# Kernel tuning notes

Hardware: AMD Instinct MI355X
Metric: run time of the kernel (lower is better)

## Reference

```python
import jax, jax.numpy as jnp
import numpy as np

_CODEBOOK = np.array([
 [-1,-1,-1,-1,-1,-1,-1,-1,-1,-1],[-1,-1,-1,-1,1,1,-1,-1,-1,1],[-1,-1,-1,1,-1,-1,-1,-1,1,1],[-1,-1,-1,1,1,1,-1,-1,1,-1],
 [-1,-1,1,-1,-1,-1,-1,1,1,-1],[-1,-1,1,-1,1,1,-1,1,1,1],[-1,-1,1,1,-1,-1,-1,1,-1,1],[-1,-1,1,1,1,1,-1,1,-1,-1],
 [-1,1,-1,-1,-1,-1,1,1,-1,-1],[-1,1,-1,-1,1,1,1,1,-1,1],[-1,1,-1,1,-1,-1,1,1,1,1],[-1,1,-1,1,1,1,1,1,1,-1],
 [-1,1,1,-1,-1,-1,1,-1,1,-1],[-1,1,1,-1,1,1,1,-1,1,1],[-1,1,1,1,-1,-1,1,-1,-1,1],[-1,1,1,1,1,1,1,-1,-1,-1],
 [1,-1,-1,-1,-1,1,1,-1,-1,-1],[1,-1,-1,-1,1,-1,1,-1,-1,1],[1,-1,-1,1,-1,1,1,-1,1,1],[1,-1,-1,1,1,-1,1,-1,1,-1],
 [1,-1,1,-1,-1,1,1,1,1,-1],[1,-1,1,-1,1,-1,1,1,1,1],[1,-1,1,1,-1,1,1,1,-1,1],[1,-1,1,1,1,-1,1,1,-1,-1],
 [1,1,-1,-1,-1,1,-1,1,-1,-1],[1,1,-1,-1,1,-1,-1,1,-1,1],[1,1,-1,1,-1,1,-1,1,1,1],[1,1,-1,1,1,-1,-1,1,1,-1],
 [1,1,1,-1,-1,1,-1,-1,1,-1],[1,1,1,-1,1,-1,-1,-1,1,1],[1,1,1,1,-1,1,-1,-1,-1,1],[1,1,1,1,1,-1,-1,-1,-1,-1]],
 dtype=np.float32)

def setup_inputs() -> dict:
    key = jax.random.key(0)
    B, N, D = 64, 65536, 10
    signal = jax.random.normal(key, (B, N, D), dtype=jnp.float32)
    codebook = jnp.asarray(_CODEBOOK)  # [32, 10]
    return {"signal": signal, "codebook": codebook}

def reference(signal, codebook):
    # Euclidean distances to all 32 codewords via Gram trick: [B, N, 32]
    x2 = jnp.sum(signal * signal, axis=-1, keepdims=True)          # [B, N, 1]
    c2 = jnp.sum(codebook * codebook, axis=-1)                      # [32]
    xc = jnp.einsum('bnd,kd->bnk', signal, codebook)                # [B, N, 32]
    d2 = jnp.maximum(x2 + c2 - 2.0 * xc, 0.0)
    distances = jnp.sqrt(d2)
    soft_assignments = jax.nn.softmax(-distances, axis=2)           # [B, N, 32]
    most_like = jnp.argmax(soft_assignments, axis=2)                # [B, N]
    softdecision = codebook[most_like]                              # [B, N, 10]
    return softdecision
```

## Files before the change

kernel.cpp:

```cpp
#include <hip/hip_runtime.h>
#include <stdint.h>

#define PTS    256
#define DIM    10
#define STRIDE 11
#define NVEC   ((PTS * DIM) / 4)

__device__ constexpr float CB[32][10] = {
 {-1,-1,-1,-1,-1,-1,-1,-1,-1,-1},{-1,-1,-1,-1,1,1,-1,-1,-1,1},{-1,-1,-1,1,-1,-1,-1,-1,1,1},{-1,-1,-1,1,1,1,-1,-1,1,-1},
 {-1,-1,1,-1,-1,-1,-1,1,1,-1},{-1,-1,1,-1,1,1,-1,1,1,1},{-1,-1,1,1,-1,-1,-1,1,-1,1},{-1,-1,1,1,1,1,-1,1,-1,-1},
 {-1,1,-1,-1,-1,-1,1,1,-1,-1},{-1,1,-1,-1,1,1,1,1,-1,1},{-1,1,-1,1,-1,-1,1,1,1,1},{-1,1,-1,1,1,1,1,1,1,-1},
 {-1,1,1,-1,-1,-1,1,-1,1,-1},{-1,1,1,-1,1,1,1,-1,1,1},{-1,1,1,1,-1,-1,1,-1,-1,1},{-1,1,1,1,1,1,1,-1,-1,-1},
 {1,-1,-1,-1,-1,1,1,-1,-1,-1},{1,-1,-1,-1,1,-1,1,-1,-1,1},{1,-1,-1,1,-1,1,1,-1,1,1},{1,-1,-1,1,1,-1,1,-1,1,-1},
 {1,-1,1,-1,-1,1,1,1,1,-1},{1,-1,1,-1,1,-1,1,1,1,1},{1,-1,1,1,-1,1,1,1,-1,1},{1,-1,1,1,1,-1,1,1,-1,-1},
 {1,1,-1,-1,-1,1,-1,1,-1,-1},{1,1,-1,-1,1,-1,-1,1,-1,1},{1,1,-1,1,-1,1,-1,1,1,1},{1,1,-1,1,1,-1,-1,1,1,-1},
 {1,1,1,-1,-1,1,-1,-1,1,-1},{1,1,1,-1,1,-1,-1,-1,1,1},{1,1,1,1,-1,1,-1,-1,-1,1},{1,1,1,1,1,-1,-1,-1,-1,-1}};

__global__ __launch_bounds__(PTS) void softdec_kernel(
    const float* __restrict__ sig, float* __restrict__ out)
{
    __shared__ float sIn [PTS * STRIDE];
    __shared__ float sOut[PTS * STRIDE];
    const int tid = threadIdx.x;
    const size_t base = (size_t)blockIdx.x * (PTS * DIM);

    const float4* __restrict__ gin = (const float4*)(sig + base);
    #pragma unroll
    for (int it = 0; it < 3; ++it) {
        const int i = tid + it * PTS;
        if (i < NVEC) {
            const float4 v = gin[i];
            const float vv[4] = {v.x, v.y, v.z, v.w};
            #pragma unroll
            for (int j = 0; j < 4; ++j) {
                const int gg = i * 4 + j;
                const int p  = gg / DIM;
                const int c  = gg - p * DIM;
                sIn[p * STRIDE + c] = vv[j];
            }
        }
    }
    __syncthreads();

    float x[DIM];
    #pragma unroll
    for (int j = 0; j < DIM; ++j) x[j] = sIn[tid * STRIDE + j];

    float best = -1e30f;
    int   bi   = 0;
    #pragma unroll
    for (int k = 0; k < 32; ++k) {
        float s = 0.0f;
        #pragma unroll
        for (int j = 0; j < DIM; ++j)
            s = (CB[k][j] > 0.0f) ? (s + x[j]) : (s - x[j]);
        if (s > best) { best = s; bi = k; }
    }

    #pragma unroll
    for (int j = 0; j < DIM; ++j)
        sOut[tid * STRIDE + j] = CB[bi][j];
    __syncthreads();

    float4* __restrict__ gout = (float4*)(out + base);
    #pragma unroll
    for (int it = 0; it < 3; ++it) {
        const int i = tid + it * PTS;
        if (i < NVEC) {
            float4 v;
            float* vv = (float*)&v;
            #pragma unroll
            for (int j = 0; j < 4; ++j) {
                const int gg = i * 4 + j;
                const int p  = gg / DIM;
                const int c  = gg - p * DIM;
                vv[j] = sOut[p * STRIDE + c];
            }
            gout[i] = v;
        }
    }
}

extern "C" void kernel_launch(void* const* d_in, const int* in_sizes, int n_in,
                              void* d_out, int out_size, void* d_ws, size_t ws_size,
                              hipStream_t stream) {
    const float* sig = (const float*)d_in[0];
    float* out = (float*)d_out;
    const int total  = in_sizes[0];
    const int pts    = total / DIM;
    const int blocks = pts / PTS;
    softdec_kernel<<<blocks, PTS, 0, stream>>>(sig, out);
}
```

Before: 278.2 us.

## Replace brute-force codeword search with factored decoder and direct vector loads

Replaces the 32x10 sign-sum search with a factored decoder that shares partial sums across codewords. It evaluates 16 candidate pairs and resolves the last bit with an absolute value and sign test. Each thread now processes two points with five 16-byte loads and stores straight from registers, removing the LDS staging buffers and both barriers. The per-thread strided vector accesses may coalesce less well than the old layout, and the result relies on the codebook's specific structure.

Measured after the change: 284.7 us. +2.4%, slower.

```diff
diff --git a/kernel.cpp b/kernel.cpp
--- a/kernel.cpp
+++ b/kernel.cpp
@@ -1,84 +1,101 @@
 #include <hip/hip_runtime.h>
 #include <stdint.h>
 
-#define PTS    256
-#define DIM    10
-#define STRIDE 11
-#define NVEC   ((PTS * DIM) / 4)
+#define THREADS 256
+#define DIM     10
 
-__device__ constexpr float CB[32][10] = {
- {-1,-1,-1,-1,-1,-1,-1,-1,-1,-1},{-1,-1,-1,-1,1,1,-1,-1,-1,1},{-1,-1,-1,1,-1,-1,-1,-1,1,1},{-1,-1,-1,1,1,1,-1,-1,1,-1},
- {-1,-1,1,-1,-1,-1,-1,1,1,-1},{-1,-1,1,-1,1,1,-1,1,1,1},{-1,-1,1,1,-1,-1,-1,1,-1,1},{-1,-1,1,1,1,1,-1,1,-1,-1},
- {-1,1,-1,-1,-1,-1,1,1,-1,-1},{-1,1,-1,-1,1,1,1,1,-1,1},{-1,1,-1,1,-1,-1,1,1,1,1},{-1,1,-1,1,1,1,1,1,1,-1},
- {-1,1,1,-1,-1,-1,1,-1,1,-1},{-1,1,1,-1,1,1,1,-1,1,1},{-1,1,1,1,-1,-1,1,-1,-1,1},{-1,1,1,1,1,1,1,-1,-1,-1},
- {1,-1,-1,-1,-1,1,1,-1,-1,-1},{1,-1,-1,-1,1,-1,1,-1,-1,1},{1,-1,-1,1,-1,1,1,-1,1,1},{1,-1,-1,1,1,-1,1,-1,1,-1},
- {1,-1,1,-1,-1,1,1,1,1,-1},{1,-1,1,-1,1,-1,1,1,1,1},{1,-1,1,1,-1,1,1,1,-1,1},{1,-1,1,1,1,-1,1,1,-1,-1},
- {1,1,-1,-1,-1,1,-1,1,-1,-1},{1,1,-1,-1,1,-1,-1,1,-1,1},{1,1,-1,1,-1,1,-1,1,1,1},{1,1,-1,1,1,-1,-1,1,1,-1},
- {1,1,1,-1,-1,1,-1,-1,1,-1},{1,1,1,-1,1,-1,-1,-1,1,1},{1,1,1,1,-1,1,-1,-1,-1,1},{1,1,1,1,1,-1,-1,-1,-1,-1}};
+typedef float v4f __attribute__((ext_vector_type(4)));
 
-__global__ __launch_bounds__(PTS) void softdec_kernel(
+
+__device__ __forceinline__ void decide10(const float* __restrict__ x,
+                                         float* __restrict__ y)
+{
+    const float x0=x[0], x1=x[1], x2=x[2], x3=x[3], x4=x[4];
+    const float x5=x[5], x6=x[6], x7=x[7], x8=x[8], x9=x[9];
+
+    const float GP = x1 - x7, GM = x1 + x7;
+    const float JP = x2 - x8, JM = x2 + x8;
+    const float LP = x3 - x9, LM = x3 + x9;
+
+    const float K11 =  LP + x4;
+    const float K10 =  LM - x4;
+    const float K01 =  x4 - LP;
+    const float K00 = -LM - x4;
+
+    const float H111 = JP + K11, H110 = JP + K10, H101 = JM + K01, H100 = JM + K00;
+    const float H011 = K11 - JP, H010 = K10 - JP, H001 = K01 - JM, H000 = K00 - JM;
+
+    float r[16];
+    r[15] = GP + H111; r[14] = GP + H110; r[13] = GP + H101; r[12] = GP + H100;
+    r[11] = GM + H011; r[10] = GM + H010; r[ 9] = GM + H001; r[ 8] = GM + H000;
+    r[ 7] = H111 - GP; r[ 6] = H110 - GP; r[ 5] = H101 - GP; r[ 4] = H100 - GP;
+    r[ 3] = H011 - GM; r[ 2] = H010 - GM; r[ 1] = H001 - GM; r[ 0] = H000 - GM;
+
+    const float p56 = x5 + x6, m56 = x5 - x6;
+    const float S11 = x0 - p56;
+    const float S10 = x0 + m56;
+    const float S01 = x0 - m56;
+    const float S00 = x0 + p56;
+    const float A11 = fabsf(S11), A10 = fabsf(S10), A01 = fabsf(S01), A00 = fabsf(S00);
+
+    float m[16];
+    #pragma unroll
+    for (int i = 0; i < 16; ++i) {
+        const bool b3 = (i >> 3) & 1, b0 = i & 1;
+        const float A = b3 ? (b0 ? A11 : A10) : (b0 ? A01 : A00);
+        m[i] = r[i] + A;
+    }
+
+    float best = m[0];
+    int   bi   = 0;
+    #pragma unroll
+    for (int i = 1; i < 16; ++i) {
+        const bool c = m[i] > best;
+        best = c ? m[i] : best;
+        bi   = c ? i    : bi;
+    }
+
+    const int wb3 = (bi >> 3) & 1, wb0 = bi & 1;
+    const float Sw = wb3 ? (wb0 ? S11 : S10) : (wb0 ? S01 : S00);
+    const float s4 = (Sw > 0.0f) ? 1.0f : -1.0f;
+    const float s0 = (bi & 1) ? 1.0f : -1.0f;
+    const float s1 = (bi & 2) ? 1.0f : -1.0f;
+    const float s2 = (bi & 4) ? 1.0f : -1.0f;
+    const float s3 = (bi & 8) ? 1.0f : -1.0f;
+
+    y[0] = s4;  y[1] = s3;  y[2] = s2;  y[3] = s1;  y[4] = s0;
+    y[5] = -s0 * s4;  y[6] = -s3 * s4;  y[7] = -s2 * s3;
+    y[8] = -s1 * s2;  y[9] = -s0 * s1;
+}
+
+__global__ __launch_bounds__(THREADS) void softdec_kernel(
     const float* __restrict__ sig, float* __restrict__ out)
 {
-    __shared__ float sIn [PTS * STRIDE];
-    __shared__ float sOut[PTS * STRIDE];
-    const int tid = threadIdx.x;
-    const size_t base = (size_t)blockIdx.x * (PTS * DIM);
+    const size_t t = (size_t)blockIdx.x * THREADS + threadIdx.x;
+    const v4f* __restrict__ gin  = (const v4f*)sig + t * 5;
+    v4f*       __restrict__ gout = (v4f*)out       + t * 5;
 
-    const float4* __restrict__ gin = (const float4*)(sig + base);
-    #pragma unroll
-    for (int it = 0; it < 3; ++it) {
-        const int i = tid + it * PTS;
-        if (i < NVEC) {
-            const float4 v = gin[i];
-            const float vv[4] = {v.x, v.y, v.z, v.w};
-            #pragma unroll
-            for (int j = 0; j < 4; ++j) {
-                const int gg = i * 4 + j;
-                const int p  = gg / DIM;
-                const int c  = gg - p * DIM;
-                sIn[p * STRIDE + c] = vv[j];
-            }
-        }
-    }
-    __syncthreads();
+    const v4f a0 = gin[0], a1 = gin[1], a2 = gin[2], a3 = gin[3], a4 = gin[4];
 
-    float x[DIM];
-    #pragma unroll
-    for (int j = 0; j < DIM; ++j) x[j] = sIn[tid * STRIDE + j];
+    float x[20];
+    x[ 0]=a0[0]; x[ 1]=a0[1]; x[ 2]=a0[2]; x[ 3]=a0[3];
+    x[ 4]=a1[0]; x[ 5]=a1[1]; x[ 6]=a1[2]; x[ 7]=a1[3];
+    x[ 8]=a2[0]; x[ 9]=a2[1]; x[10]=a2[2]; x[11]=a2[3];
+    x[12]=a3[0]; x[13]=a3[1]; x[14]=a3[2]; x[15]=a3[3];
+    x[16]=a4[0]; x[17]=a4[1]; x[18]=a4[2]; x[19]=a4[3];
 
-    float best = -1e30f;
-    int   bi   = 0;
-    #pragma unroll
-    for (int k = 0; k < 32; ++k) {
-        float s = 0.0f;
-        #pragma unroll
-        for (int j = 0; j < DIM; ++j)
-            s = (CB[k][j] > 0.0f) ? (s + x[j]) : (s - x[j]);
-        if (s > best) { best = s; bi = k; }
-    }
+    float y[20];
+    decide10(x,      y);
+    decide10(x + 10, y + 10);
 
-    #pragma unroll
-    for (int j = 0; j < DIM; ++j)
-        sOut[tid * STRIDE + j] = CB[bi][j];
-    __syncthreads();
+    v4f o0, o1, o2, o3, o4;
+    o0[0]=y[ 0]; o0[1]=y[ 1]; o0[2]=y[ 2]; o0[3]=y[ 3];
+    o1[0]=y[ 4]; o1[1]=y[ 5]; o1[2]=y[ 6]; o1[3]=y[ 7];
+    o2[0]=y[ 8]; o2[1]=y[ 9]; o2[2]=y[10]; o2[3]=y[11];
+    o3[0]=y[12]; o3[1]=y[13]; o3[2]=y[14]; o3[3]=y[15];
+    o4[0]=y[16]; o4[1]=y[17]; o4[2]=y[18]; o4[3]=y[19];
 
-    float4* __restrict__ gout = (float4*)(out + base);
-    #pragma unroll
-    for (int it = 0; it < 3; ++it) {
-        const int i = tid + it * PTS;
-        if (i < NVEC) {
-            float4 v;
-            float* vv = (float*)&v;
-            #pragma unroll
-            for (int j = 0; j < 4; ++j) {
-                const int gg = i * 4 + j;
-                const int p  = gg / DIM;
-                const int c  = gg - p * DIM;
-                vv[j] = sOut[p * STRIDE + c];
-            }
-            gout[i] = v;
-        }
-    }
+    gout[0] = o0; gout[1] = o1; gout[2] = o2; gout[3] = o3; gout[4] = o4;
 }
 
 extern "C" void kernel_launch(void* const* d_in, const int* in_sizes, int n_in,
@@ -86,8 +103,9 @@
                               hipStream_t stream) {
     const float* sig = (const float*)d_in[0];
     float* out = (float*)d_out;
-    const int total  = in_sizes[0];
-    const int pts    = total / DIM;
-    const int blocks = pts / PTS;
-    softdec_kernel<<<blocks, PTS, 0, stream>>>(sig, out);
+    const int total   = in_sizes[0];
+    const int pts     = total / DIM;
+    const int threads = pts / 2;
+    const int blocks  = threads / THREADS;
+    softdec_kernel<<<blocks, THREADS, 0, stream>>>(sig, out);
 }
```
